# Performance work log

Hardware: AMD Instinct MI355X
Metric: run time of the kernel (lower is better)

## Reference

```python
import jax, jax.numpy as jnp
import numpy as np

B, CIN, COUT, H, W = 8, 128, 256, 64, 64
EPS = 1e-5


def conv2d(x, w, b, pad):
    y = jax.lax.conv_general_dilated(
        x, w, window_strides=(1, 1), padding=[(pad, pad), (pad, pad)],
        dimension_numbers=('NCHW', 'OIHW', 'NCHW'))
    return y + b[None, :, None, None]


def deform_sample(x, offset):
    # x: [B,C,H,W], offset: [B,18,H,W] -> sampled: [B,C,9,H,W]
    b, c, h, w = x.shape
    off = offset.reshape(b, 9, 2, h, w)  # (dy, dx) per kernel tap (torchvision v1 order)
    ky = (jnp.arange(9) // 3 - 1).astype(x.dtype)
    kx = (jnp.arange(9) % 3 - 1).astype(x.dtype)
    py = jnp.arange(h, dtype=x.dtype)[None, None, :, None] + ky[None, :, None, None] + off[:, :, 0]
    px = jnp.arange(w, dtype=x.dtype)[None, None, None, :] + kx[None, :, None, None] + off[:, :, 1]
    y0 = jnp.floor(py); x0 = jnp.floor(px)
    fy = py - y0;       fx = px - x0
    xf = x.reshape(b, c, h * w)

    def gather(iy, ix):
        valid = (iy >= 0) & (iy < h) & (ix >= 0) & (ix < w)
        iyc = jnp.clip(iy, 0, h - 1).astype(jnp.int32)
        ixc = jnp.clip(ix, 0, w - 1).astype(jnp.int32)
        idx = (iyc * w + ixc).reshape(b, -1)  # [B, 9*H*W]
        g = jax.vmap(lambda xb, ib: jnp.take(xb, ib, axis=1))(xf, idx)  # [B,C,9HW]
        return g.reshape(b, c, 9, h, w) * valid.astype(x.dtype)[:, None]

    samp = (gather(y0,     x0    ) * ((1 - fy) * (1 - fx))[:, None]
          + gather(y0,     x0 + 1) * ((1 - fy) * fx      )[:, None]
          + gather(y0 + 1, x0    ) * (fy * (1 - fx)      )[:, None]
          + gather(y0 + 1, x0 + 1) * (fy * fx            )[:, None])
    return samp


def setup_inputs():
    key = jax.random.key(0)
    ks = jax.random.split(key, 8)
    return {
        'x':     jax.random.normal(ks[0], (B, CIN, H, W), jnp.float32),
        'w_off': jax.random.normal(ks[1], (18, CIN, 3, 3), jnp.float32) * 0.01,
        'b_off': jnp.zeros((18,), jnp.float32),
        'w_def': jax.random.normal(ks[2], (COUT, CIN, 3, 3), jnp.float32) * 0.03,
        'b_def': jax.random.normal(ks[3], (COUT,), jnp.float32) * 0.01,
        'gamma': jnp.ones((COUT,), jnp.float32),
        'beta':  jnp.zeros((COUT,), jnp.float32),
        'w_sc':  jax.random.normal(ks[4], (COUT, CIN, 1, 1), jnp.float32) * 0.05,
        'b_sc':  jnp.zeros((COUT,), jnp.float32),
    }


def reference(x, w_off, b_off, w_def, b_def, gamma, beta, w_sc, b_sc):
    offset = conv2d(x, w_off, b_off, pad=1)                 # [B,18,H,W]
    samp = deform_sample(x, offset)                         # [B,C,9,H,W]
    out = jnp.einsum('bckhw,ock->bohw', samp, w_def.reshape(COUT, CIN, 9))
    out = out + b_def[None, :, None, None]
    # BatchNorm2d (training mode: batch statistics)
    mean = out.mean(axis=(0, 2, 3))
    var = out.var(axis=(0, 2, 3))
    out = (out - mean[None, :, None, None]) * jax.lax.rsqrt(var + EPS)[None, :, None, None]
    out = out * gamma[None, :, None, None] + beta[None, :, None, None]
    out = out + conv2d(x, w_sc, b_sc, pad=0)                # residual shortcut (1x1)
    return jax.nn.relu(out)
```

## Files before the change

### kernel.cpp

```cpp
#include <hip/hip_runtime.h>

typedef __attribute__((ext_vector_type(8))) short bf16x8;
typedef __attribute__((ext_vector_type(4))) float f32x4;

__device__ __forceinline__ float bf2f(unsigned short u) {
  return __uint_as_float(((unsigned int)u) << 16);
}
__device__ __forceinline__ unsigned short f2bf(float f) {
  unsigned int u = __float_as_uint(f);
  u += 0x7fffu + ((u >> 16) & 1u);
  return (unsigned short)(u >> 16);
}

constexpr size_t OFF_XPAD = 0;
constexpr size_t SZ_XPAD  = (size_t)8 * 66 * 66 * 128 * 2;
constexpr size_t OFF_WB   = OFF_XPAD + SZ_XPAD;
constexpr size_t SZ_WB    = (size_t)9 * 16 * 256 * 8 * 2;
constexpr size_t OFF_WS2  = OFF_WB + SZ_WB;
constexpr size_t SZ_WS2   = (size_t)16 * 256 * 8 * 2;
constexpr size_t OFF_WO   = OFF_WS2 + SZ_WS2;
constexpr size_t SZ_WO    = (size_t)9 * 16 * 32 * 8 * 2;
constexpr size_t OFF_YM   = OFF_WO + SZ_WO;
constexpr size_t SZ_YM    = (size_t)32768 * 256 * 2;
constexpr size_t OFF_PART = OFF_YM + SZ_YM;
constexpr size_t SZ_PART  = (size_t)512 * 256 * 2 * 4;
constexpr size_t OFF_STAT = OFF_PART + SZ_PART;

__global__ __launch_bounds__(256) void k_prep_x(const float* __restrict__ x,
                                                unsigned short* __restrict__ xp) {
  int blk = blockIdx.x;
  int b = blk >> 6, h = blk & 63;
  int t = threadIdx.x;
  __shared__ float tile[16][66];
  for (int cc = 0; cc < 8; ++cc) {
    int c0 = cc * 16;
    int wr = t & 63, cl = t >> 6;
#pragma unroll
    for (int i = 0; i < 4; ++i) {
      int c = c0 + cl * 4 + i;
      tile[cl * 4 + i][wr] = x[(((size_t)b * 128 + c) * 64 + h) * 64 + wr];
    }
    __syncthreads();
    int ww = t >> 2, cq = t & 3;
    ushort4 u4;
    u4.x = f2bf(tile[cq * 4 + 0][ww]);
    u4.y = f2bf(tile[cq * 4 + 1][ww]);
    u4.z = f2bf(tile[cq * 4 + 2][ww]);
    u4.w = f2bf(tile[cq * 4 + 3][ww]);
    *(ushort4*)(xp + ((size_t)(b * 66 + h + 1) * 66 + (ww + 1)) * 128 + c0 + cq * 4) = u4;
    __syncthreads();
  }
}

__global__ __launch_bounds__(256) void k_pack_w(const float* __restrict__ wdef,
                                                const float* __restrict__ wsc,
                                                const float* __restrict__ woff,
                                                unsigned short* __restrict__ wB,
                                                unsigned short* __restrict__ wS,
                                                unsigned short* __restrict__ wO) {
  int tid = blockIdx.x * 256 + threadIdx.x;
  if (tid < 294912) {
    int k8 = tid & 7, n = (tid >> 3) & 255, kb = (tid >> 11) & 15, tap = tid >> 15;
    int c = kb * 8 + k8;
    wB[tid] = f2bf(wdef[((size_t)n * 128 + c) * 9 + tap]);
  } else if (tid < 294912 + 32768) {
    int i = tid - 294912;
    int k8 = i & 7, n = (i >> 3) & 255, kb = i >> 11;
    wS[i] = f2bf(wsc[(size_t)n * 128 + kb * 8 + k8]);
  } else if (tid < 294912 + 32768 + 36864) {
    int i = tid - 327680;
    int k8 = i & 7, n = (i >> 3) & 31, kb = (i >> 8) & 15, tap = i >> 12;
    int c = kb * 8 + k8;
    wO[i] = f2bf(n < 18 ? woff[((size_t)n * 128 + c) * 9 + tap] : 0.f);
  }
}

__global__ __launch_bounds__(256) void k_main(const unsigned short* __restrict__ xp,
                                              const unsigned short* __restrict__ wB,
                                              const unsigned short* __restrict__ wO,
                                              const float* __restrict__ boff,
                                              const float* __restrict__ bdef,
                                              unsigned short* __restrict__ ymain,
                                              float* __restrict__ partials) {
  int blk = blockIdx.x;
  int b = blk >> 6, h = blk & 63;
  int t = threadIdx.x;
  int lane = t & 63, wid = t >> 6;
  int m = lane & 15, quad = lane >> 4;
  __shared__ __align__(16) unsigned short At[2][64 * 136];
  __shared__ float offsL[9][64][2];

  {
    f32x4 a0 = {0.f, 0.f, 0.f, 0.f}, a1 = {0.f, 0.f, 0.f, 0.f};
    int px = wid * 16 + m;
    const unsigned short* xbase = xp + ((size_t)(b * 66 + h) * 66 + px) * 128 + quad * 8;
    for (int tap = 0; tap < 9; ++tap) {
      const unsigned short* arow = xbase + ((tap / 3) * 66 + (tap % 3)) * 128;
#pragma unroll
      for (int kk = 0; kk < 4; ++kk) {
        bf16x8 a = *(const bf16x8*)(arow + kk * 32);
        const unsigned short* bb = wO + (size_t)(tap * 16 + kk * 4 + quad) * 256;
        bf16x8 b0 = *(const bf16x8*)(bb + m * 8);
        bf16x8 b1 = *(const bf16x8*)(bb + (16 + m) * 8);
        a0 = __builtin_amdgcn_mfma_f32_16x16x32_bf16(a, b0, a0, 0, 0, 0);
        a1 = __builtin_amdgcn_mfma_f32_16x16x32_bf16(a, b1, a1, 0, 0, 0);
      }
    }
#pragma unroll
    for (int r = 0; r < 4; ++r) {
      int pxs = wid * 16 + quad * 4 + r;
      offsL[m >> 1][pxs][m & 1] = a0[r] + boff[m];
      if (m < 2) offsL[8][pxs][m] = a1[r] + boff[16 + m];
    }
  }
  __syncthreads();

  f32x4 acc[4][4];
#pragma unroll
  for (int i = 0; i < 4; ++i)
#pragma unroll
    for (int j = 0; j < 4; ++j) acc[i][j] = (f32x4){0.f, 0.f, 0.f, 0.f};

  int px_s = t >> 2, sub = t & 3;
  const unsigned short* xb_base = xp + (size_t)b * 66 * 66 * 128;
  int nb = wid * 64;

  auto sample_prep = [&](int tap, float* wgt, const unsigned short** p) {
    float2 ov = *(const float2*)&offsL[tap][px_s][0];
    int ky = tap / 3 - 1, kx = tap % 3 - 1;
    float py = (float)(h + ky) + ov.x;
    float pxf = (float)(px_s + kx) + ov.y;
    float y0f = floorf(py), x0f = floorf(pxf);
    float fy = py - y0f, fx = pxf - x0f;
    int iy0 = (int)y0f, ix0 = (int)x0f;
#pragma unroll
    for (int j = 0; j < 4; ++j) {
      int iy = iy0 + (j >> 1), ix = ix0 + (j & 1);
      float wy = (j >> 1) ? fy : 1.f - fy;
      float wx = (j & 1) ? fx : 1.f - fx;
      bool valid = (iy >= 0) && (iy < 64) && (ix >= 0) && (ix < 64);
      int iyc = min(max(iy, 0), 63), ixc = min(max(ix, 0), 63);
      wgt[j] = valid ? wy * wx : 0.f;
      p[j] = xb_base + ((size_t)(iyc + 1) * 66 + (ixc + 1)) * 128 + sub * 8;
    }
  };
  auto load_g2 = [&](const unsigned short** p, int g0, bf16x8 (*v)[4]) {
#pragma unroll
    for (int gg = 0; gg < 2; ++gg)
#pragma unroll
      for (int j = 0; j < 4; ++j)
        v[gg][j] = *(const bf16x8*)(p[j] + (g0 + gg) * 32);
  };
  auto store_g2 = [&](unsigned short* dst, int g0, const float* wgt, bf16x8 (*v)[4]) {
#pragma unroll
    for (int gg = 0; gg < 2; ++gg) {
      bf16x8 o;
#pragma unroll
      for (int j = 0; j < 8; ++j) {
        float s = fmaf(wgt[0], bf2f((unsigned short)v[gg][0][j]),
                  fmaf(wgt[1], bf2f((unsigned short)v[gg][1][j]),
                  fmaf(wgt[2], bf2f((unsigned short)v[gg][2][j]),
                       wgt[3] * bf2f((unsigned short)v[gg][3][j]))));
        o[j] = (short)f2bf(s);
      }
      *(bf16x8*)(dst + (g0 + gg) * 32) = o;
    }
  };
  auto mfma_half = [&](const unsigned short* buf, int tap, int kk0) {
#pragma unroll
    for (int kk = kk0; kk < kk0 + 2; ++kk) {
      bf16x8 af[4];
#pragma unroll
      for (int ms = 0; ms < 4; ++ms)
        af[ms] = *(const bf16x8*)(buf + (ms * 16 + m) * 136 + kk * 32 + quad * 8);
#pragma unroll
      for (int ns = 0; ns < 4; ++ns) {
        bf16x8 bfr = *(const bf16x8*)(wB + ((size_t)(tap * 16 + kk * 4 + quad) * 256 + nb + ns * 16 + m) * 8);
#pragma unroll
        for (int ms = 0; ms < 4; ++ms)
          acc[ms][ns] = __builtin_amdgcn_mfma_f32_16x16x32_bf16(af[ms], bfr, acc[ms][ns], 0, 0, 0);
      }
    }
  };

  {
    float wgt[4]; const unsigned short* p[4]; bf16x8 v[2][4];
    sample_prep(0, wgt, p);
    unsigned short* dst = &At[0][px_s * 136 + sub * 8];
    load_g2(p, 0, v); store_g2(dst, 0, wgt, v);
    load_g2(p, 2, v); store_g2(dst, 2, wgt, v);
  }
#pragma unroll
  for (int tap = 0; tap < 9; ++tap) {
    __syncthreads();
    const unsigned short* cur = At[tap & 1];
    unsigned short* dst = &At[(tap + 1) & 1][px_s * 136 + sub * 8];
    if (tap < 8) {
      float wgt[4]; const unsigned short* p[4]; bf16x8 v[2][4];
      sample_prep(tap + 1, wgt, p);
      load_g2(p, 0, v);
      mfma_half(cur, tap, 0);
      store_g2(dst, 0, wgt, v);
      load_g2(p, 2, v);
      mfma_half(cur, tap, 2);
      store_g2(dst, 2, wgt, v);
    } else {
      mfma_half(cur, tap, 0);
      mfma_half(cur, tap, 2);
    }
  }

  __syncthreads();
  unsigned short* yb = &At[0][0];
#pragma unroll
  for (int ns = 0; ns < 4; ++ns) {
    int n = nb + ns * 16 + m;
    float bias = bdef[n];
    float s = 0.f, q = 0.f;
#pragma unroll
    for (int ms = 0; ms < 4; ++ms) {
#pragma unroll
      for (int r = 0; r < 4; ++r) {
        int px = ms * 16 + quad * 4 + r;
        float v = acc[ms][ns][r] + bias;
        yb[px * 264 + n] = f2bf(v);
        s += v;
        q += v * v;
      }
    }
    s += __shfl_xor(s, 16); s += __shfl_xor(s, 32);
    q += __shfl_xor(q, 16); q += __shfl_xor(q, 32);
    if (quad == 0) {
      partials[((size_t)blk * 256 + n) * 2 + 0] = s;
      partials[((size_t)blk * 256 + n) * 2 + 1] = q;
    }
  }
  __syncthreads();
  {
    unsigned short* grow = ymain + (size_t)(blk * 64 + px_s) * 256;
    const unsigned short* lrow = yb + px_s * 264;
#pragma unroll
    for (int k = 0; k < 8; ++k) {
      int n0 = k * 32 + sub * 8;
      *(bf16x8*)(grow + n0) = *(const bf16x8*)(lrow + n0);
    }
  }
}

__global__ __launch_bounds__(64) void k_stats(const float* __restrict__ partials,
                                              const float* __restrict__ gamma,
                                              const float* __restrict__ beta,
                                              float* __restrict__ stats) {
  int ch = blockIdx.x;
  int L = threadIdx.x;
  float s = 0.f, q = 0.f;
#pragma unroll
  for (int i = 0; i < 8; ++i) {
    int row = i * 64 + L;
    s += partials[((size_t)row * 256 + ch) * 2 + 0];
    q += partials[((size_t)row * 256 + ch) * 2 + 1];
  }
#pragma unroll
  for (int d = 1; d < 64; d <<= 1) { s += __shfl_xor(s, d); q += __shfl_xor(q, d); }
  if (L == 0) {
    float mean = s * (1.f / 32768.f);
    float var = q * (1.f / 32768.f) - mean * mean;
    float inv = rsqrtf(var + 1e-5f);
    float A = gamma[ch] * inv;
    stats[ch * 2 + 0] = A;
    stats[ch * 2 + 1] = beta[ch] - mean * A;
  }
}

__global__ __launch_bounds__(256) void k_final(const unsigned short* __restrict__ xp,
                                               const unsigned short* __restrict__ wS,
                                               const unsigned short* __restrict__ ymain,
                                               const float* __restrict__ stats,
                                               const float* __restrict__ bsc,
                                               float* __restrict__ out) {
  int blk = blockIdx.x;
  int b = blk >> 6, h = blk & 63;
  int t = threadIdx.x;
  int lane = t & 63, wid = t >> 6;
  int m = lane & 15, quad = lane >> 4;
  __shared__ float tr[128 * 67];
  f32x4 acc[4][4];
#pragma unroll
  for (int i = 0; i < 4; ++i)
#pragma unroll
    for (int j = 0; j < 4; ++j) acc[i][j] = (f32x4){0.f, 0.f, 0.f, 0.f};
  const unsigned short* xrow = xp + ((size_t)(b * 66 + h + 1) * 66 + 1) * 128;
  int nb = wid * 64;
#pragma unroll
  for (int kk = 0; kk < 4; ++kk) {
    bf16x8 af[4];
#pragma unroll
    for (int ms = 0; ms < 4; ++ms)
      af[ms] = *(const bf16x8*)(xrow + (ms * 16 + m) * 128 + kk * 32 + quad * 8);
#pragma unroll
    for (int ns = 0; ns < 4; ++ns) {
      bf16x8 bfr = *(const bf16x8*)(wS + ((size_t)(kk * 4 + quad) * 256 + nb + ns * 16 + m) * 8);
#pragma unroll
      for (int ms = 0; ms < 4; ++ms)
        acc[ms][ns] = __builtin_amdgcn_mfma_f32_16x16x32_bf16(af[ms], bfr, acc[ms][ns], 0, 0, 0);
    }
  }
  for (int pass = 0; pass < 2; ++pass) {
    if ((wid >> 1) == pass) {
#pragma unroll
      for (int ns = 0; ns < 4; ++ns) {
        int n = nb + ns * 16 + m;
        float bs = bsc[n];
        int nl = n - pass * 128;
#pragma unroll
        for (int ms = 0; ms < 4; ++ms)
#pragma unroll
          for (int r = 0; r < 4; ++r) {
            int px = ms * 16 + quad * 4 + r;
            tr[nl * 67 + px] = acc[ms][ns][r] + bs;
          }
      }
    }
    __syncthreads();
    {
      int nl = t & 127, g = t >> 7;
      int n = pass * 128 + nl;
      float A = stats[n * 2], Bc = stats[n * 2 + 1];
#pragma unroll 8
      for (int i = 0; i < 32; ++i) {
        int px = g * 32 + i;
        float ym = bf2f(ymain[(size_t)(blk * 64 + px) * 256 + n]);
        float* pt = &tr[nl * 67 + px];
        *pt = fmaxf(fmaf(ym, A, Bc) + *pt, 0.f);
      }
    }
    __syncthreads();
    {
      int ww = t & 63, ng = t >> 6;
#pragma unroll 8
      for (int i = 0; i < 32; ++i) {
        int nl = ng * 32 + i;
        out[((size_t)(b * 256 + pass * 128 + nl) * 64 + h) * 64 + ww] = tr[nl * 67 + ww];
      }
    }
    __syncthreads();
  }
}

extern "C" void kernel_launch(void* const* d_in, const int* in_sizes, int n_in,
                              void* d_out, int out_size, void* d_ws, size_t ws_size,
                              hipStream_t stream) {
  const float* x     = (const float*)d_in[0];
  const float* w_off = (const float*)d_in[1];
  const float* b_off = (const float*)d_in[2];
  const float* w_def = (const float*)d_in[3];
  const float* b_def = (const float*)d_in[4];
  const float* gamma = (const float*)d_in[5];
  const float* beta  = (const float*)d_in[6];
  const float* w_sc  = (const float*)d_in[7];
  const float* b_sc  = (const float*)d_in[8];
  float* out = (float*)d_out;

  char* ws = (char*)d_ws;
  unsigned short* xpad  = (unsigned short*)(ws + OFF_XPAD);
  unsigned short* wB    = (unsigned short*)(ws + OFF_WB);
  unsigned short* wS    = (unsigned short*)(ws + OFF_WS2);
  unsigned short* wO    = (unsigned short*)(ws + OFF_WO);
  unsigned short* ymain = (unsigned short*)(ws + OFF_YM);
  float* partials       = (float*)(ws + OFF_PART);
  float* stats          = (float*)(ws + OFF_STAT);

  hipMemsetAsync(xpad, 0, SZ_XPAD, stream);
  k_prep_x<<<512, 256, 0, stream>>>(x, xpad);
  k_pack_w<<<1424, 256, 0, stream>>>(w_def, w_sc, w_off, wB, wS, wO);
  k_main<<<512, 256, 0, stream>>>(xpad, wB, wO, b_off, b_def, ymain, partials);
  k_stats<<<256, 64, 0, stream>>>(partials, gamma, beta, stats);
  k_final<<<512, 256, 0, stream>>>(xpad, wS, ymain, stats, b_sc, out);
}
```

Baseline: 162.1 us.

## Split rows into half-row blocks, transpose ymain layout, drop LDS transpose in final

Each block now handles 32 pixels instead of a full 64-pixel row, doubling the grid to 1024 blocks in prep, main and final, with launch bounds requesting 4 blocks per CU. ymain is stored channel-major so the final kernel can compute the shortcut GEMM with swapped operands and write NCHW output directly from registers, removing the shared-memory transpose. The sampling loop now issues all gathers per tap at once, and the stats reduction handles twice as many partials. The trade-off is less reuse per block (the offset conv uses only two waves) and strided scalar stores of ymain.

```diff
diff --git a/kernel.cpp b/kernel.cpp
--- a/kernel.cpp
+++ b/kernel.cpp
@@ -21,19 +21,19 @@
 constexpr size_t OFF_WO   = OFF_WS2 + SZ_WS2;
 constexpr size_t SZ_WO    = (size_t)9 * 16 * 32 * 8 * 2;
 constexpr size_t OFF_YM   = OFF_WO + SZ_WO;
-constexpr size_t SZ_YM    = (size_t)32768 * 256 * 2;
+constexpr size_t SZ_YM    = (size_t)256 * 32768 * 2;
 constexpr size_t OFF_PART = OFF_YM + SZ_YM;
-constexpr size_t SZ_PART  = (size_t)512 * 256 * 2 * 4;
+constexpr size_t SZ_PART  = (size_t)1024 * 256 * 2 * 4;
 constexpr size_t OFF_STAT = OFF_PART + SZ_PART;
 
 __global__ __launch_bounds__(256) void k_prep_x(const float* __restrict__ x,
                                                 unsigned short* __restrict__ xp) {
   int blk = blockIdx.x;
-  int b = blk >> 6, h = blk & 63;
+  int b = blk >> 7, h = (blk >> 1) & 63, chalf = blk & 1;
   int t = threadIdx.x;
   __shared__ float tile[16][66];
-  for (int cc = 0; cc < 8; ++cc) {
-    int c0 = cc * 16;
+  for (int cc = 0; cc < 4; ++cc) {
+    int c0 = (chalf * 4 + cc) * 16;
     int wr = t & 63, cl = t >> 6;
 #pragma unroll
     for (int i = 0; i < 4; ++i) {
@@ -75,25 +75,26 @@
   }
 }
 
-__global__ __launch_bounds__(256) void k_main(const unsigned short* __restrict__ xp,
-                                              const unsigned short* __restrict__ wB,
-                                              const unsigned short* __restrict__ wO,
-                                              const float* __restrict__ boff,
-                                              const float* __restrict__ bdef,
-                                              unsigned short* __restrict__ ymain,
-                                              float* __restrict__ partials) {
+__global__ __launch_bounds__(256, 4) void k_main(const unsigned short* __restrict__ xp,
+                                                 const unsigned short* __restrict__ wB,
+                                                 const unsigned short* __restrict__ wO,
+                                                 const float* __restrict__ boff,
+                                                 const float* __restrict__ bdef,
+                                                 unsigned short* __restrict__ ymain,
+                                                 float* __restrict__ partials) {
   int blk = blockIdx.x;
-  int b = blk >> 6, h = blk & 63;
+  int b = blk >> 7, h = (blk >> 1) & 63, half = blk & 1;
+  int px0 = half * 32;
   int t = threadIdx.x;
   int lane = t & 63, wid = t >> 6;
   int m = lane & 15, quad = lane >> 4;
-  __shared__ __align__(16) unsigned short At[2][64 * 136];
-  __shared__ float offsL[9][64][2];
-
-  {
+  __shared__ __align__(16) unsigned short At[2][32 * 136];
+  __shared__ float offsL[9][32][2];
+
+  if (wid < 2) {
     f32x4 a0 = {0.f, 0.f, 0.f, 0.f}, a1 = {0.f, 0.f, 0.f, 0.f};
     int px = wid * 16 + m;
-    const unsigned short* xbase = xp + ((size_t)(b * 66 + h) * 66 + px) * 128 + quad * 8;
+    const unsigned short* xbase = xp + ((size_t)(b * 66 + h) * 66 + px0 + px) * 128 + quad * 8;
     for (int tap = 0; tap < 9; ++tap) {
       const unsigned short* arow = xbase + ((tap / 3) * 66 + (tap % 3)) * 128;
 #pragma unroll
@@ -115,13 +116,13 @@
   }
   __syncthreads();
 
-  f32x4 acc[4][4];
-#pragma unroll
-  for (int i = 0; i < 4; ++i)
+  f32x4 acc[2][4];
+#pragma unroll
+  for (int i = 0; i < 2; ++i)
 #pragma unroll
     for (int j = 0; j < 4; ++j) acc[i][j] = (f32x4){0.f, 0.f, 0.f, 0.f};
 
-  int px_s = t >> 2, sub = t & 3;
+  int px_s = t >> 3, sub = t & 7;
   const unsigned short* xb_base = xp + (size_t)b * 66 * 66 * 128;
   int nb = wid * 64;
 
@@ -129,7 +130,7 @@
     float2 ov = *(const float2*)&offsL[tap][px_s][0];
     int ky = tap / 3 - 1, kx = tap % 3 - 1;
     float py = (float)(h + ky) + ov.x;
-    float pxf = (float)(px_s + kx) + ov.y;
+    float pxf = (float)(px0 + px_s + kx) + ov.y;
     float y0f = floorf(py), x0f = floorf(pxf);
     float fy = py - y0f, fx = pxf - x0f;
     int iy0 = (int)y0f, ix0 = (int)x0f;
@@ -144,40 +145,40 @@
       p[j] = xb_base + ((size_t)(iyc + 1) * 66 + (ixc + 1)) * 128 + sub * 8;
     }
   };
-  auto load_g2 = [&](const unsigned short** p, int g0, bf16x8 (*v)[4]) {
-#pragma unroll
-    for (int gg = 0; gg < 2; ++gg)
+  auto load_all = [&](const unsigned short** p, bf16x8 (*v)[4]) {
+#pragma unroll
+    for (int g = 0; g < 2; ++g)
 #pragma unroll
       for (int j = 0; j < 4; ++j)
-        v[gg][j] = *(const bf16x8*)(p[j] + (g0 + gg) * 32);
+        v[g][j] = *(const bf16x8*)(p[j] + g * 64);
   };
-  auto store_g2 = [&](unsigned short* dst, int g0, const float* wgt, bf16x8 (*v)[4]) {
-#pragma unroll
-    for (int gg = 0; gg < 2; ++gg) {
+  auto store_all = [&](unsigned short* dst, const float* wgt, bf16x8 (*v)[4]) {
+#pragma unroll
+    for (int g = 0; g < 2; ++g) {
       bf16x8 o;
 #pragma unroll
       for (int j = 0; j < 8; ++j) {
-        float s = fmaf(wgt[0], bf2f((unsigned short)v[gg][0][j]),
-                  fmaf(wgt[1], bf2f((unsigned short)v[gg][1][j]),
-                  fmaf(wgt[2], bf2f((unsigned short)v[gg][2][j]),
-                       wgt[3] * bf2f((unsigned short)v[gg][3][j]))));
+        float s = fmaf(wgt[0], bf2f((unsigned short)v[g][0][j]),
+                  fmaf(wgt[1], bf2f((unsigned short)v[g][1][j]),
+                  fmaf(wgt[2], bf2f((unsigned short)v[g][2][j]),
+                       wgt[3] * bf2f((unsigned short)v[g][3][j]))));
         o[j] = (short)f2bf(s);
       }
-      *(bf16x8*)(dst + (g0 + gg) * 32) = o;
+      *(bf16x8*)(dst + g * 64) = o;
     }
   };
-  auto mfma_half = [&](const unsigned short* buf, int tap, int kk0) {
-#pragma unroll
-    for (int kk = kk0; kk < kk0 + 2; ++kk) {
-      bf16x8 af[4];
-#pragma unroll
-      for (int ms = 0; ms < 4; ++ms)
+  auto mfma_tap = [&](const unsigned short* buf, int tap) {
+#pragma unroll
+    for (int kk = 0; kk < 4; ++kk) {
+      bf16x8 af[2];
+#pragma unroll
+      for (int ms = 0; ms < 2; ++ms)
         af[ms] = *(const bf16x8*)(buf + (ms * 16 + m) * 136 + kk * 32 + quad * 8);
 #pragma unroll
       for (int ns = 0; ns < 4; ++ns) {
         bf16x8 bfr = *(const bf16x8*)(wB + ((size_t)(tap * 16 + kk * 4 + quad) * 256 + nb + ns * 16 + m) * 8);
 #pragma unroll
-        for (int ms = 0; ms < 4; ++ms)
+        for (int ms = 0; ms < 2; ++ms)
           acc[ms][ns] = __builtin_amdgcn_mfma_f32_16x16x32_bf16(af[ms], bfr, acc[ms][ns], 0, 0, 0);
       }
     }
@@ -186,27 +187,21 @@
   {
     float wgt[4]; const unsigned short* p[4]; bf16x8 v[2][4];
     sample_prep(0, wgt, p);
-    unsigned short* dst = &At[0][px_s * 136 + sub * 8];
-    load_g2(p, 0, v); store_g2(dst, 0, wgt, v);
-    load_g2(p, 2, v); store_g2(dst, 2, wgt, v);
+    load_all(p, v);
+    store_all(&At[0][px_s * 136 + sub * 8], wgt, v);
   }
 #pragma unroll
   for (int tap = 0; tap < 9; ++tap) {
     __syncthreads();
     const unsigned short* cur = At[tap & 1];
-    unsigned short* dst = &At[(tap + 1) & 1][px_s * 136 + sub * 8];
     if (tap < 8) {
       float wgt[4]; const unsigned short* p[4]; bf16x8 v[2][4];
       sample_prep(tap + 1, wgt, p);
-      load_g2(p, 0, v);
-      mfma_half(cur, tap, 0);
-      store_g2(dst, 0, wgt, v);
-      load_g2(p, 2, v);
-      mfma_half(cur, tap, 2);
-      store_g2(dst, 2, wgt, v);
+      load_all(p, v);
+      mfma_tap(cur, tap);
+      store_all(&At[(tap + 1) & 1][px_s * 136 + sub * 8], wgt, v);
     } else {
-      mfma_half(cur, tap, 0);
-      mfma_half(cur, tap, 2);
+      mfma_tap(cur, tap);
     }
   }
 
@@ -218,12 +213,12 @@
     float bias = bdef[n];
     float s = 0.f, q = 0.f;
 #pragma unroll
-    for (int ms = 0; ms < 4; ++ms) {
+    for (int ms = 0; ms < 2; ++ms) {
 #pragma unroll
       for (int r = 0; r < 4; ++r) {
         int px = ms * 16 + quad * 4 + r;
         float v = acc[ms][ns][r] + bias;
-        yb[px * 264 + n] = f2bf(v);
+        yb[px * 258 + n] = f2bf(v);
         s += v;
         q += v * v;
       }
@@ -237,12 +232,13 @@
   }
   __syncthreads();
   {
-    unsigned short* grow = ymain + (size_t)(blk * 64 + px_s) * 256;
-    const unsigned short* lrow = yb + px_s * 264;
-#pragma unroll
-    for (int k = 0; k < 8; ++k) {
-      int n0 = k * 32 + sub * 8;
-      *(bf16x8*)(grow + n0) = *(const bf16x8*)(lrow + n0);
+    int px_l = t & 31, n_g = t >> 5;
+    const unsigned short* col = yb + px_l * 258;
+    unsigned short* gdst = ymain + blk * 32 + px_l;
+#pragma unroll
+    for (int i = 0; i < 32; ++i) {
+      int n = n_g * 32 + i;
+      gdst[(size_t)n * 32768] = col[n];
     }
   }
 }
@@ -255,7 +251,7 @@
   int L = threadIdx.x;
   float s = 0.f, q = 0.f;
 #pragma unroll
-  for (int i = 0; i < 8; ++i) {
+  for (int i = 0; i < 16; ++i) {
     int row = i * 64 + L;
     s += partials[((size_t)row * 256 + ch) * 2 + 0];
     q += partials[((size_t)row * 256 + ch) * 2 + 1];
@@ -272,78 +268,53 @@
   }
 }
 
-__global__ __launch_bounds__(256) void k_final(const unsigned short* __restrict__ xp,
-                                               const unsigned short* __restrict__ wS,
-                                               const unsigned short* __restrict__ ymain,
-                                               const float* __restrict__ stats,
-                                               const float* __restrict__ bsc,
-                                               float* __restrict__ out) {
+__global__ __launch_bounds__(256, 4) void k_final(const unsigned short* __restrict__ xp,
+                                                  const unsigned short* __restrict__ wS,
+                                                  const unsigned short* __restrict__ ymain,
+                                                  const float* __restrict__ stats,
+                                                  const float* __restrict__ bsc,
+                                                  float* __restrict__ out) {
   int blk = blockIdx.x;
-  int b = blk >> 6, h = blk & 63;
+  int b = blk >> 7, h = (blk >> 1) & 63, half = blk & 1;
   int t = threadIdx.x;
   int lane = t & 63, wid = t >> 6;
   int m = lane & 15, quad = lane >> 4;
-  __shared__ float tr[128 * 67];
-  f32x4 acc[4][4];
+  f32x4 acc[4][2];
 #pragma unroll
   for (int i = 0; i < 4; ++i)
 #pragma unroll
-    for (int j = 0; j < 4; ++j) acc[i][j] = (f32x4){0.f, 0.f, 0.f, 0.f};
-  const unsigned short* xrow = xp + ((size_t)(b * 66 + h + 1) * 66 + 1) * 128;
+    for (int j = 0; j < 2; ++j) acc[i][j] = (f32x4){0.f, 0.f, 0.f, 0.f};
+  const unsigned short* xrow = xp + ((size_t)(b * 66 + h + 1) * 66 + 1 + half * 32) * 128;
   int nb = wid * 64;
 #pragma unroll
   for (int kk = 0; kk < 4; ++kk) {
-    bf16x8 af[4];
-#pragma unroll
-    for (int ms = 0; ms < 4; ++ms)
-      af[ms] = *(const bf16x8*)(xrow + (ms * 16 + m) * 128 + kk * 32 + quad * 8);
-#pragma unroll
-    for (int ns = 0; ns < 4; ++ns) {
-      bf16x8 bfr = *(const bf16x8*)(wS + ((size_t)(kk * 4 + quad) * 256 + nb + ns * 16 + m) * 8);
-#pragma unroll
-      for (int ms = 0; ms < 4; ++ms)
-        acc[ms][ns] = __builtin_amdgcn_mfma_f32_16x16x32_bf16(af[ms], bfr, acc[ms][ns], 0, 0, 0);
-    }
-  }
-  for (int pass = 0; pass < 2; ++pass) {
-    if ((wid >> 1) == pass) {
-#pragma unroll
-      for (int ns = 0; ns < 4; ++ns) {
-        int n = nb + ns * 16 + m;
-        float bs = bsc[n];
-        int nl = n - pass * 128;
-#pragma unroll
-        for (int ms = 0; ms < 4; ++ms)
-#pragma unroll
-          for (int r = 0; r < 4; ++r) {
-            int px = ms * 16 + quad * 4 + r;
-            tr[nl * 67 + px] = acc[ms][ns][r] + bs;
-          }
-      }
-    }
-    __syncthreads();
-    {
-      int nl = t & 127, g = t >> 7;
-      int n = pass * 128 + nl;
-      float A = stats[n * 2], Bc = stats[n * 2 + 1];
-#pragma unroll 8
-      for (int i = 0; i < 32; ++i) {
-        int px = g * 32 + i;
-        float ym = bf2f(ymain[(size_t)(blk * 64 + px) * 256 + n]);
-        float* pt = &tr[nl * 67 + px];
-        *pt = fmaxf(fmaf(ym, A, Bc) + *pt, 0.f);
-      }
-    }
-    __syncthreads();
-    {
-      int ww = t & 63, ng = t >> 6;
-#pragma unroll 8
-      for (int i = 0; i < 32; ++i) {
-        int nl = ng * 32 + i;
-        out[((size_t)(b * 256 + pass * 128 + nl) * 64 + h) * 64 + ww] = tr[nl * 67 + ww];
-      }
-    }
-    __syncthreads();
+    bf16x8 xf[2];
+#pragma unroll
+    for (int pt = 0; pt < 2; ++pt)
+      xf[pt] = *(const bf16x8*)(xrow + (pt * 16 + m) * 128 + kk * 32 + quad * 8);
+#pragma unroll
+    for (int ct = 0; ct < 4; ++ct) {
+      bf16x8 wf = *(const bf16x8*)(wS + ((size_t)(kk * 4 + quad) * 256 + nb + ct * 16 + m) * 8);
+#pragma unroll
+      for (int pt = 0; pt < 2; ++pt)
+        acc[ct][pt] = __builtin_amdgcn_mfma_f32_16x16x32_bf16(wf, xf[pt], acc[ct][pt], 0, 0, 0);
+    }
+  }
+#pragma unroll
+  for (int ct = 0; ct < 4; ++ct) {
+#pragma unroll
+    for (int r = 0; r < 4; ++r) {
+      int ch = nb + ct * 16 + quad * 4 + r;
+      float A = stats[ch * 2], Bc = stats[ch * 2 + 1];
+      float bs = bsc[ch] + Bc;
+#pragma unroll
+      for (int pt = 0; pt < 2; ++pt) {
+        int px = pt * 16 + m;
+        float ym = bf2f(ymain[(size_t)ch * 32768 + blk * 32 + px]);
+        float v = fmaxf(fmaf(ym, A, bs) + acc[ct][pt][r], 0.f);
+        out[(((size_t)(b * 256 + ch) * 64 + h) * 64) + half * 32 + px] = v;
+      }
+    }
   }
 }
 
@@ -371,9 +342,9 @@
   float* stats          = (float*)(ws + OFF_STAT);
 
   hipMemsetAsync(xpad, 0, SZ_XPAD, stream);
-  k_prep_x<<<512, 256, 0, stream>>>(x, xpad);
+  k_prep_x<<<1024, 256, 0, stream>>>(x, xpad);
   k_pack_w<<<1424, 256, 0, stream>>>(w_def, w_sc, w_off, wB, wS, wO);
-  k_main<<<512, 256, 0, stream>>>(xpad, wB, wO, b_off, b_def, ymain, partials);
+  k_main<<<1024, 256, 0, stream>>>(xpad, wB, wO, b_off, b_def, ymain, partials);
   k_stats<<<256, 64, 0, stream>>>(partials, gamma, beta, stats);
-  k_final<<<512, 256, 0, stream>>>(xpad, wS, ymain, stats, b_sc, out);
-}
+  k_final<<<1024, 256, 0, stream>>>(xpad, wS, ymain, stats, b_sc, out);
+}
```

Result: no change. 165.1 us (+1.8%).

## Split main and final kernels across channel halves and store ymain channel-major

Applied to the files above, without the earlier changes.

Merges the x-pack and weight-pack kernels into one launch. Splits k_main into two blocks per row, one per half of the output channels, to double the grid; each block recomputes the offset conv and the bilinear sampling. Stores the intermediate ymain channel-major so that k_final can apply BN, add the residual and apply ReLU straight from MFMA registers, with no LDS transpose, over 2048 smaller blocks. The cost is the offset and sampling work done twice in k_main, and narrower global stores in the final kernel.

```diff
diff --git a/kernel.cpp b/kernel.cpp
--- a/kernel.cpp
+++ b/kernel.cpp
@@ -1,4 +1,5 @@
 #include <hip/hip_runtime.h>
+#include <hip/hip_bf16.h>
 
 typedef __attribute__((ext_vector_type(8))) short bf16x8;
 typedef __attribute__((ext_vector_type(4))) float f32x4;
@@ -21,57 +22,58 @@
 constexpr size_t OFF_WO   = OFF_WS2 + SZ_WS2;
 constexpr size_t SZ_WO    = (size_t)9 * 16 * 32 * 8 * 2;
 constexpr size_t OFF_YM   = OFF_WO + SZ_WO;
-constexpr size_t SZ_YM    = (size_t)32768 * 256 * 2;
+constexpr size_t SZ_YM    = (size_t)256 * 32768 * 2;
 constexpr size_t OFF_PART = OFF_YM + SZ_YM;
 constexpr size_t SZ_PART  = (size_t)512 * 256 * 2 * 4;
 constexpr size_t OFF_STAT = OFF_PART + SZ_PART;
 
-__global__ __launch_bounds__(256) void k_prep_x(const float* __restrict__ x,
-                                                unsigned short* __restrict__ xp) {
+__global__ __launch_bounds__(256) void k_prep(const float* __restrict__ x,
+                                              const float* __restrict__ wdef,
+                                              const float* __restrict__ wsc,
+                                              const float* __restrict__ woff,
+                                              unsigned short* __restrict__ xp,
+                                              unsigned short* __restrict__ wB,
+                                              unsigned short* __restrict__ wS,
+                                              unsigned short* __restrict__ wO) {
   int blk = blockIdx.x;
-  int b = blk >> 6, h = blk & 63;
   int t = threadIdx.x;
-  __shared__ float tile[16][66];
-  for (int cc = 0; cc < 8; ++cc) {
-    int c0 = cc * 16;
-    int wr = t & 63, cl = t >> 6;
-#pragma unroll
-    for (int i = 0; i < 4; ++i) {
-      int c = c0 + cl * 4 + i;
-      tile[cl * 4 + i][wr] = x[(((size_t)b * 128 + c) * 64 + h) * 64 + wr];
-    }
-    __syncthreads();
-    int ww = t >> 2, cq = t & 3;
-    ushort4 u4;
-    u4.x = f2bf(tile[cq * 4 + 0][ww]);
-    u4.y = f2bf(tile[cq * 4 + 1][ww]);
-    u4.z = f2bf(tile[cq * 4 + 2][ww]);
-    u4.w = f2bf(tile[cq * 4 + 3][ww]);
-    *(ushort4*)(xp + ((size_t)(b * 66 + h + 1) * 66 + (ww + 1)) * 128 + c0 + cq * 4) = u4;
-    __syncthreads();
-  }
-}
-
-__global__ __launch_bounds__(256) void k_pack_w(const float* __restrict__ wdef,
-                                                const float* __restrict__ wsc,
-                                                const float* __restrict__ woff,
-                                                unsigned short* __restrict__ wB,
-                                                unsigned short* __restrict__ wS,
-                                                unsigned short* __restrict__ wO) {
-  int tid = blockIdx.x * 256 + threadIdx.x;
-  if (tid < 294912) {
-    int k8 = tid & 7, n = (tid >> 3) & 255, kb = (tid >> 11) & 15, tap = tid >> 15;
-    int c = kb * 8 + k8;
-    wB[tid] = f2bf(wdef[((size_t)n * 128 + c) * 9 + tap]);
-  } else if (tid < 294912 + 32768) {
-    int i = tid - 294912;
-    int k8 = i & 7, n = (i >> 3) & 255, kb = i >> 11;
-    wS[i] = f2bf(wsc[(size_t)n * 128 + kb * 8 + k8]);
-  } else if (tid < 294912 + 32768 + 36864) {
-    int i = tid - 327680;
-    int k8 = i & 7, n = (i >> 3) & 31, kb = (i >> 8) & 15, tap = i >> 12;
-    int c = kb * 8 + k8;
-    wO[i] = f2bf(n < 18 ? woff[((size_t)n * 128 + c) * 9 + tap] : 0.f);
+  if (blk < 1024) {
+    int b = blk >> 7, h = (blk >> 1) & 63, chalf = blk & 1;
+    __shared__ float tile[16][66];
+    for (int cc = 0; cc < 4; ++cc) {
+      int c0 = (chalf * 4 + cc) * 16;
+      int wr = t & 63, cl = t >> 6;
+#pragma unroll
+      for (int i = 0; i < 4; ++i) {
+        int c = c0 + cl * 4 + i;
+        tile[cl * 4 + i][wr] = x[(((size_t)b * 128 + c) * 64 + h) * 64 + wr];
+      }
+      __syncthreads();
+      int ww = t >> 2, cq = t & 3;
+      ushort4 u4;
+      u4.x = f2bf(tile[cq * 4 + 0][ww]);
+      u4.y = f2bf(tile[cq * 4 + 1][ww]);
+      u4.z = f2bf(tile[cq * 4 + 2][ww]);
+      u4.w = f2bf(tile[cq * 4 + 3][ww]);
+      *(ushort4*)(xp + ((size_t)(b * 66 + h + 1) * 66 + (ww + 1)) * 128 + c0 + cq * 4) = u4;
+      __syncthreads();
+    }
+  } else {
+    int tid = (blk - 1024) * 256 + t;
+    if (tid < 294912) {
+      int k8 = tid & 7, n = (tid >> 3) & 255, kb = (tid >> 11) & 15, tap = tid >> 15;
+      int c = kb * 8 + k8;
+      wB[tid] = f2bf(wdef[((size_t)n * 128 + c) * 9 + tap]);
+    } else if (tid < 294912 + 32768) {
+      int i = tid - 294912;
+      int k8 = i & 7, n = (i >> 3) & 255, kb = i >> 11;
+      wS[i] = f2bf(wsc[(size_t)n * 128 + kb * 8 + k8]);
+    } else if (tid < 294912 + 32768 + 36864) {
+      int i = tid - 327680;
+      int k8 = i & 7, n = (i >> 3) & 31, kb = (i >> 8) & 15, tap = i >> 12;
+      int c = kb * 8 + k8;
+      wO[i] = f2bf(n < 18 ? woff[((size_t)n * 128 + c) * 9 + tap] : 0.f);
+    }
   }
 }
 
@@ -83,7 +85,8 @@
                                               unsigned short* __restrict__ ymain,
                                               float* __restrict__ partials) {
   int blk = blockIdx.x;
-  int b = blk >> 6, h = blk & 63;
+  int rowtile = blk >> 1, nhalf = blk & 1;
+  int b = rowtile >> 6, h = rowtile & 63;
   int t = threadIdx.x;
   int lane = t & 63, wid = t >> 6;
   int m = lane & 15, quad = lane >> 4;
@@ -115,15 +118,15 @@
   }
   __syncthreads();
 
-  f32x4 acc[4][4];
+  f32x4 acc[4][2];
 #pragma unroll
   for (int i = 0; i < 4; ++i)
 #pragma unroll
-    for (int j = 0; j < 4; ++j) acc[i][j] = (f32x4){0.f, 0.f, 0.f, 0.f};
+    for (int j = 0; j < 2; ++j) acc[i][j] = (f32x4){0.f, 0.f, 0.f, 0.f};
 
   int px_s = t >> 2, sub = t & 3;
   const unsigned short* xb_base = xp + (size_t)b * 66 * 66 * 128;
-  int nb = wid * 64;
+  int nb = nhalf * 128 + wid * 32;
 
   auto sample_prep = [&](int tap, float* wgt, const unsigned short** p) {
     float2 ov = *(const float2*)&offsL[tap][px_s][0];
@@ -174,7 +177,7 @@
       for (int ms = 0; ms < 4; ++ms)
         af[ms] = *(const bf16x8*)(buf + (ms * 16 + m) * 136 + kk * 32 + quad * 8);
 #pragma unroll
-      for (int ns = 0; ns < 4; ++ns) {
+      for (int ns = 0; ns < 2; ++ns) {
         bf16x8 bfr = *(const bf16x8*)(wB + ((size_t)(tap * 16 + kk * 4 + quad) * 256 + nb + ns * 16 + m) * 8);
 #pragma unroll
         for (int ms = 0; ms < 4; ++ms)
@@ -213,36 +216,39 @@
   __syncthreads();
   unsigned short* yb = &At[0][0];
 #pragma unroll
-  for (int ns = 0; ns < 4; ++ns) {
+  for (int ns = 0; ns < 2; ++ns) {
     int n = nb + ns * 16 + m;
+    int nl = n - nhalf * 128;
     float bias = bdef[n];
     float s = 0.f, q = 0.f;
 #pragma unroll
     for (int ms = 0; ms < 4; ++ms) {
-#pragma unroll
-      for (int r = 0; r < 4; ++r) {
-        int px = ms * 16 + quad * 4 + r;
-        float v = acc[ms][ns][r] + bias;
-        yb[px * 264 + n] = f2bf(v);
-        s += v;
-        q += v * v;
-      }
+      ushort4 u;
+      float v0 = acc[ms][ns][0] + bias;
+      float v1 = acc[ms][ns][1] + bias;
+      float v2 = acc[ms][ns][2] + bias;
+      float v3 = acc[ms][ns][3] + bias;
+      u.x = f2bf(v0); u.y = f2bf(v1); u.z = f2bf(v2); u.w = f2bf(v3);
+      *(ushort4*)(yb + nl * 68 + ms * 16 + quad * 4) = u;
+      s += v0 + v1 + v2 + v3;
+      q += v0 * v0 + v1 * v1 + v2 * v2 + v3 * v3;
     }
     s += __shfl_xor(s, 16); s += __shfl_xor(s, 32);
     q += __shfl_xor(q, 16); q += __shfl_xor(q, 32);
     if (quad == 0) {
-      partials[((size_t)blk * 256 + n) * 2 + 0] = s;
-      partials[((size_t)blk * 256 + n) * 2 + 1] = q;
+      partials[((size_t)rowtile * 256 + n) * 2 + 0] = s;
+      partials[((size_t)rowtile * 256 + n) * 2 + 1] = q;
     }
   }
   __syncthreads();
   {
-    unsigned short* grow = ymain + (size_t)(blk * 64 + px_s) * 256;
-    const unsigned short* lrow = yb + px_s * 264;
-#pragma unroll
-    for (int k = 0; k < 8; ++k) {
-      int n0 = k * 32 + sub * 8;
-      *(bf16x8*)(grow + n0) = *(const bf16x8*)(lrow + n0);
+    int px2 = t & 31, n_g = t >> 5;
+    unsigned int* ymu = (unsigned int*)ymain;
+#pragma unroll
+    for (int i = 0; i < 16; ++i) {
+      int nl = n_g * 16 + i;
+      unsigned int v = *(const unsigned int*)(yb + nl * 68 + px2 * 2);
+      ymu[((size_t)(nhalf * 128 + nl) * 32768 + rowtile * 64) / 2 + px2] = v;
     }
   }
 }
@@ -279,71 +285,46 @@
                                                const float* __restrict__ bsc,
                                                float* __restrict__ out) {
   int blk = blockIdx.x;
-  int b = blk >> 6, h = blk & 63;
+  int chalf = blk & 1, half = (blk >> 1) & 1, h = (blk >> 2) & 63, b = blk >> 8;
+  int rowblk = blk >> 1;
   int t = threadIdx.x;
   int lane = t & 63, wid = t >> 6;
   int m = lane & 15, quad = lane >> 4;
-  __shared__ float tr[128 * 67];
-  f32x4 acc[4][4];
-#pragma unroll
-  for (int i = 0; i < 4; ++i)
-#pragma unroll
-    for (int j = 0; j < 4; ++j) acc[i][j] = (f32x4){0.f, 0.f, 0.f, 0.f};
-  const unsigned short* xrow = xp + ((size_t)(b * 66 + h + 1) * 66 + 1) * 128;
-  int nb = wid * 64;
+  f32x4 acc[2][2];
+#pragma unroll
+  for (int i = 0; i < 2; ++i)
+#pragma unroll
+    for (int j = 0; j < 2; ++j) acc[i][j] = (f32x4){0.f, 0.f, 0.f, 0.f};
+  const unsigned short* xrow = xp + ((size_t)(b * 66 + h + 1) * 66 + 1 + half * 32) * 128;
+  int nb = chalf * 128 + wid * 32;
 #pragma unroll
   for (int kk = 0; kk < 4; ++kk) {
-    bf16x8 af[4];
-#pragma unroll
-    for (int ms = 0; ms < 4; ++ms)
-      af[ms] = *(const bf16x8*)(xrow + (ms * 16 + m) * 128 + kk * 32 + quad * 8);
-#pragma unroll
-    for (int ns = 0; ns < 4; ++ns) {
-      bf16x8 bfr = *(const bf16x8*)(wS + ((size_t)(kk * 4 + quad) * 256 + nb + ns * 16 + m) * 8);
-#pragma unroll
-      for (int ms = 0; ms < 4; ++ms)
-        acc[ms][ns] = __builtin_amdgcn_mfma_f32_16x16x32_bf16(af[ms], bfr, acc[ms][ns], 0, 0, 0);
-    }
-  }
-  for (int pass = 0; pass < 2; ++pass) {
-    if ((wid >> 1) == pass) {
-#pragma unroll
-      for (int ns = 0; ns < 4; ++ns) {
-        int n = nb + ns * 16 + m;
-        float bs = bsc[n];
-        int nl = n - pass * 128;
-#pragma unroll
-        for (int ms = 0; ms < 4; ++ms)
-#pragma unroll
-          for (int r = 0; r < 4; ++r) {
-            int px = ms * 16 + quad * 4 + r;
-            tr[nl * 67 + px] = acc[ms][ns][r] + bs;
-          }
-      }
-    }
-    __syncthreads();
-    {
-      int nl = t & 127, g = t >> 7;
-      int n = pass * 128 + nl;
-      float A = stats[n * 2], Bc = stats[n * 2 + 1];
-#pragma unroll 8
-      for (int i = 0; i < 32; ++i) {
-        int px = g * 32 + i;
-        float ym = bf2f(ymain[(size_t)(blk * 64 + px) * 256 + n]);
-        float* pt = &tr[nl * 67 + px];
-        *pt = fmaxf(fmaf(ym, A, Bc) + *pt, 0.f);
-      }
-    }
-    __syncthreads();
-    {
-      int ww = t & 63, ng = t >> 6;
-#pragma unroll 8
-      for (int i = 0; i < 32; ++i) {
-        int nl = ng * 32 + i;
-        out[((size_t)(b * 256 + pass * 128 + nl) * 64 + h) * 64 + ww] = tr[nl * 67 + ww];
-      }
-    }
-    __syncthreads();
+    bf16x8 xf[2];
+#pragma unroll
+    for (int pt = 0; pt < 2; ++pt)
+      xf[pt] = *(const bf16x8*)(xrow + (pt * 16 + m) * 128 + kk * 32 + quad * 8);
+#pragma unroll
+    for (int ct = 0; ct < 2; ++ct) {
+      bf16x8 wf = *(const bf16x8*)(wS + ((size_t)(kk * 4 + quad) * 256 + nb + ct * 16 + m) * 8);
+#pragma unroll
+      for (int pt = 0; pt < 2; ++pt)
+        acc[ct][pt] = __builtin_amdgcn_mfma_f32_16x16x32_bf16(wf, xf[pt], acc[ct][pt], 0, 0, 0);
+    }
+  }
+#pragma unroll
+  for (int ct = 0; ct < 2; ++ct) {
+#pragma unroll
+    for (int r = 0; r < 4; ++r) {
+      int ch = nb + ct * 16 + quad * 4 + r;
+      float A = stats[ch * 2], Bc = stats[ch * 2 + 1] + bsc[ch];
+#pragma unroll
+      for (int pt = 0; pt < 2; ++pt) {
+        int px = pt * 16 + m;
+        float ym = bf2f(ymain[(size_t)ch * 32768 + rowblk * 32 + px]);
+        float v = fmaxf(fmaf(ym, A, Bc) + acc[ct][pt][r], 0.f);
+        out[(((size_t)(b * 256 + ch) * 64 + h) * 64) + half * 32 + px] = v;
+      }
+    }
   }
 }
 
@@ -371,9 +352,8 @@
   float* stats          = (float*)(ws + OFF_STAT);
 
   hipMemsetAsync(xpad, 0, SZ_XPAD, stream);
-  k_prep_x<<<512, 256, 0, stream>>>(x, xpad);
-  k_pack_w<<<1424, 256, 0, stream>>>(w_def, w_sc, w_off, wB, wS, wO);
-  k_main<<<512, 256, 0, stream>>>(xpad, wB, wO, b_off, b_def, ymain, partials);
+  k_prep<<<2448, 256, 0, stream>>>(x, w_def, w_sc, w_off, xpad, wB, wS, wO);
+  k_main<<<1024, 256, 0, stream>>>(xpad, wB, wO, b_off, b_def, ymain, partials);
   k_stats<<<256, 64, 0, stream>>>(partials, gamma, beta, stats);
-  k_final<<<512, 256, 0, stream>>>(xpad, wS, ymain, stats, b_sc, out);
-}
+  k_final<<<2048, 256, 0, stream>>>(xpad, wS, ymain, stats, b_sc, out);
+}
```

New measurement: 184.3 us. +13.6%, slower.
